# Kernel optimization log

Measured on AMD Instinct MI355X. Metric: run time of the kernel, lower is better.

The kernel has to match this reference:

```python
import jax, jax.numpy as jnp
import numpy as np

N = 100000      # nodes
E = 1600000     # edges
F_IN = 512      # input features
H = 64          # hidden
R = 2           # relations
B = 30          # bases
NEG_SLOPE = 0.2 # GATConv default


def setup_inputs() -> dict:
    key = jax.random.key(0)
    ks = jax.random.split(key, 14)
    s_in = 1.0 / np.sqrt(F_IN)
    s_h = 1.0 / np.sqrt(H)
    return {
        "x": jax.random.normal(ks[0], (N, F_IN), jnp.float32),
        "edge_index": jax.random.randint(ks[1], (2, E), 0, N),
        "edge_types": jax.random.randint(ks[2], (E,), 0, R),
        # RGCN layer 1 (F_IN -> H), basis-decomposed
        "basis1": jax.random.normal(ks[3], (B, F_IN, H), jnp.float32) * s_in,
        "comp1": jax.random.normal(ks[4], (R, B), jnp.float32) * (1.0 / np.sqrt(B)),
        "root1": jax.random.normal(ks[5], (F_IN, H), jnp.float32) * s_in,
        "bias1": jnp.zeros((H,), jnp.float32),
        # RGCN layer 2 (H -> H)
        "basis2": jax.random.normal(ks[6], (B, H, H), jnp.float32) * s_h,
        "comp2": jax.random.normal(ks[7], (R, B), jnp.float32) * (1.0 / np.sqrt(B)),
        "root2": jax.random.normal(ks[8], (H, H), jnp.float32) * s_h,
        "bias2": jnp.zeros((H,), jnp.float32),
        # GAT (H -> 1, heads=1)
        "gat_w": jax.random.normal(ks[9], (H, 1), jnp.float32) * s_h,
        "att_src": jax.random.normal(ks[10], (1,), jnp.float32),
        "att_dst": jax.random.normal(ks[11], (1,), jnp.float32),
        "gat_bias": jnp.zeros((1,), jnp.float32),
    }


def rgcn_layer(x, src, dst, etype, basis, comp, root, bias):
    # W_r = sum_b comp[r,b] * basis[b]; transform nodes once per relation,
    # then gather per edge (math-equal to PyG's per-edge transform, cheaper).
    W = jnp.einsum('rb,bio->rio', comp, basis)       # [R, in, out]
    h = jnp.einsum('ni,rio->rno', x, W)              # [R, N, out]
    out = x @ root + bias                            # root/self term
    for r in range(R):                               # R=2, fixed small loop
        m = (etype == r).astype(x.dtype)             # [E]
        msg = h[r][src] * m[:, None]                 # gather + mask
        agg = jax.ops.segment_sum(msg, dst, num_segments=N)
        cnt = jax.ops.segment_sum(m, dst, num_segments=N)
        out = out + agg / jnp.maximum(cnt, 1.0)[:, None]   # mean aggr per relation
    return out


def gat_layer(x, src, dst, gat_w, att_src, att_dst, gat_bias):
    # GATConv with heads=1, out=1, add_self_loops=True, negative_slope=0.2
    loop = jnp.arange(N)
    s = jnp.concatenate([src, loop])
    d = jnp.concatenate([dst, loop])
    h = x @ gat_w                                    # [N, 1]
    a_s = h[:, 0] * att_src[0]                       # [N]
    a_d = h[:, 0] * att_dst[0]                       # [N]
    e = jax.nn.leaky_relu(a_s[s] + a_d[d], NEG_SLOPE)  # [E+N]
    emax = jax.ops.segment_max(e, d, num_segments=N)   # every dst has self-loop
    ex = jnp.exp(e - emax[d])
    denom = jax.ops.segment_sum(ex, d, num_segments=N)
    alpha = ex / denom[d]                            # segment softmax over dst
    out = jax.ops.segment_sum(alpha[:, None] * h[s], d, num_segments=N)
    return out + gat_bias


def reference(x, edge_index, edge_types,
              basis1, comp1, root1, bias1,
              basis2, comp2, root2, bias2,
              gat_w, att_src, att_dst, gat_bias):
    src, dst = edge_index[0], edge_index[1]
    x1 = jax.nn.relu(rgcn_layer(x, src, dst, edge_types, basis1, comp1, root1, bias1))
    x2 = rgcn_layer(x1, src, dst, edge_types, basis2, comp2, root2, bias2)
    return gat_layer(x2, src, dst, gat_w, att_src, att_dst, gat_bias)  # [N, 1]
```

## Files before the change

### kernel.cpp

```cpp
#include <hip/hip_runtime.h>
#include <hip/hip_bf16.h>
#include <math.h>

#define NCOL 192
#define BB   30
#define SCAN_T 256
#define SCAN_ELEMS 1024

typedef short bf16x8 __attribute__((ext_vector_type(8)));
typedef float f32x4  __attribute__((ext_vector_type(4)));
typedef unsigned short u16x8 __attribute__((ext_vector_type(8)));

__device__ __forceinline__ ushort f2bf(float f) {
  unsigned u = __float_as_uint(f);
  unsigned r = u + 0x7fff + ((u >> 16) & 1);
  return (ushort)(r >> 16);
}
__device__ __forceinline__ float bf2f(ushort u) {
  return __uint_as_float(((unsigned)u) << 16);
}

__global__ void zero_int(int* __restrict__ p, int n) {
  int i = blockIdx.x * blockDim.x + threadIdx.x;
  if (i < n) p[i] = 0;
}

__global__ void hist_deg(const int* __restrict__ dst, int* __restrict__ deg, int E) {
  int e = blockIdx.x * blockDim.x + threadIdx.x;
  if (e >= E) return;
  atomicAdd(&deg[dst[e]], 1);
}

__global__ __launch_bounds__(SCAN_T) void scan_local(const int* __restrict__ deg,
                                                     int* __restrict__ rowptr,
                                                     int* __restrict__ partial, int N) {
  __shared__ int sdata[SCAN_T];
  int t = threadIdx.x;
  int base = blockIdx.x * SCAN_ELEMS + t * 4;
  int v[4], s = 0;
#pragma unroll
  for (int k = 0; k < 4; ++k) {
    v[k] = (base + k < N) ? deg[base + k] : 0;
    s += v[k];
  }
  sdata[t] = s;
  __syncthreads();
  for (int off = 1; off < SCAN_T; off <<= 1) {
    int add = (t >= off) ? sdata[t - off] : 0;
    __syncthreads();
    sdata[t] += add;
    __syncthreads();
  }
  int run = sdata[t] - s;
  if (t == SCAN_T - 1) partial[blockIdx.x] = sdata[t];
#pragma unroll
  for (int k = 0; k < 4; ++k) {
    if (base + k <= N) rowptr[base + k] = run;
    run += v[k];
  }
}

__global__ __launch_bounds__(SCAN_T) void scan_partial(int* __restrict__ partial, int nb) {
  __shared__ int sdata[SCAN_T];
  int t = threadIdx.x;
  int v = (t < nb) ? partial[t] : 0;
  sdata[t] = v;
  __syncthreads();
  for (int off = 1; off < SCAN_T; off <<= 1) {
    int add = (t >= off) ? sdata[t - off] : 0;
    __syncthreads();
    sdata[t] += add;
    __syncthreads();
  }
  if (t < nb) partial[t] = sdata[t] - v;
  if (t == nb - 1) partial[nb] = sdata[t];
}

__global__ void scatter_edges(const int* __restrict__ src, const int* __restrict__ dst,
                              const int* __restrict__ et, const int* __restrict__ rowptr,
                              const int* __restrict__ partial,
                              int* __restrict__ fill, int* __restrict__ srcpk, int E) {
  int e = blockIdx.x * blockDim.x + threadIdx.x;
  if (e >= E) return;
  int d = dst[e];
  int pos = rowptr[d] + partial[d >> 10] + atomicAdd(&fill[d], 1);
  srcpk[pos] = src[e] | (et[e] << 30);
}

__global__ void build_weights(const float* __restrict__ basis1, const float* __restrict__ comp1,
                              const float* __restrict__ root1,
                              const float* __restrict__ basis2, const float* __restrict__ comp2,
                              const float* __restrict__ root2,
                              const float* __restrict__ bias2, const float* __restrict__ gw,
                              ushort* __restrict__ Wpk1, float* __restrict__ w2g,
                              float* __restrict__ cb) {
  int idx = blockIdx.x * blockDim.x + threadIdx.x;
  if (idx < 512 * NCOL) {
    int k = idx / NCOL, j = idx - k * NCOL;
    float v;
    if (j < 64) {
      v = root1[k * 64 + j];
    } else {
      int r = (j >> 6) - 1, o = j & 63;
      float s = 0.f;
#pragma unroll
      for (int b = 0; b < BB; ++b)
        s = fmaf(comp1[r * BB + b], basis1[((size_t)b * 512 + k) * 64 + o], s);
      v = s;
    }
    int chunk = k >> 6, kg = (k >> 3) & 7, elem = k & 7;
    int slot = (kg * NCOL + j) ^ kg;
    Wpk1[(size_t)chunk * 12288 + slot * 8 + elem] = f2bf(v);
    return;
  }
  int widx = idx - 512 * NCOL;
  int c = widx >> 6;
  int o = widx & 63;
  if (c < 192) {
    int k = c & 63, part = c >> 6;
    float s;
    if (part == 0) {
      s = root2[k * 64 + o] * gw[o];
    } else {
      int r = part - 1;
      float t = 0.f;
#pragma unroll
      for (int b = 0; b < BB; ++b)
        t = fmaf(comp2[r * BB + b], basis2[((size_t)b * 64 + k) * 64 + o], t);
      s = t * gw[o];
    }
#pragma unroll
    for (int off = 32; off > 0; off >>= 1) s += __shfl_xor(s, off);
    if (o == 0) w2g[c] = s;
  } else if (c == 192) {
    float s = bias2[o] * gw[o];
#pragma unroll
    for (int off = 32; off > 0; off >>= 1) s += __shfl_xor(s, off);
    if (o == 0) *cb = s;
  }
}

template <int K, int BF16IN>
__global__ __launch_bounds__(256, 3) void gemm_mfma(const void* __restrict__ Xv,
                                                    const ushort* __restrict__ Wpk,
                                                    ushort* __restrict__ Y, int N) {
  constexpr int NC = K / 64;
  constexpr int NB = (NC > 1) ? 2 : 1;
  __shared__ ushort Ws[NB * 12288];

  const int tid  = threadIdx.x;
  const int wid  = tid >> 6;
  const int lane = tid & 63;
  const int lrow = lane & 15;
  const int lhi  = lane >> 4;
  const int row0 = blockIdx.x * 64 + wid * 16;

  int lr = row0 + lrow;
  if (lr >= N) lr = N - 1;
  const float*  Xf = (const float*)Xv  + (size_t)lr * K;
  const ushort* Xh = (const ushort*)Xv + (size_t)lr * K;

#define GLOAD_W(c, buf)                                                        \
  { const ushort* gsrc = Wpk + (size_t)(c) * 12288 + wid * 3072 + lane * 8;    \
    ushort* ldst = Ws + (size_t)(buf) * 12288 + wid * 3072;                    \
    _Pragma("unroll") for (int i = 0; i < 6; ++i)                              \
      __builtin_amdgcn_global_load_lds(                                        \
          (const __attribute__((address_space(1))) unsigned int*)(gsrc + i * 512), \
          (__attribute__((address_space(3))) unsigned int*)(ldst + i * 512),   \
          16, 0, 0); }

  float4 pa[2][4];
  u16x8  ph[2][2];
#define LOAD_A(c, slot)                                                       \
  if constexpr (BF16IN) {                                                     \
    ph[slot][0] = ((const u16x8*)Xh)[(c) * 8 + lhi];                          \
    ph[slot][1] = ((const u16x8*)Xh)[(c) * 8 + 4 + lhi];                      \
  } else {                                                                    \
    _Pragma("unroll") for (int q = 0; q < 4; ++q)                             \
      pa[slot][q] = ((const float4*)Xf)[(c) * 16 + (q >> 1) * 8 + lhi * 2 + (q & 1)]; \
  }
#define MAT_A(slot, tt, areg)                                                 \
  if constexpr (BF16IN) {                                                     \
    areg = (bf16x8)ph[slot][tt];                                              \
  } else {                                                                    \
    float4 v0 = pa[slot][(tt) * 2], v1 = pa[slot][(tt) * 2 + 1];              \
    areg[0] = (short)f2bf(v0.x); areg[1] = (short)f2bf(v0.y);                 \
    areg[2] = (short)f2bf(v0.z); areg[3] = (short)f2bf(v0.w);                 \
    areg[4] = (short)f2bf(v1.x); areg[5] = (short)f2bf(v1.y);                 \
    areg[6] = (short)f2bf(v1.z); areg[7] = (short)f2bf(v1.w);                 \
  }
#define COMP(buf, tt, areg)                                                   \
  { const int kg = (tt) * 4 + lhi;                                            \
    const ushort* ls = Ws + (size_t)(buf) * 12288;                            \
    _Pragma("unroll") for (int h = 0; h < 2; ++h) {                           \
      bf16x8 b[6];                                                            \
      _Pragma("unroll") for (int q = 0; q < 6; ++q) {                         \
        int slot = (kg * NCOL + (h * 6 + q) * 16 + lrow) ^ (kg & 7);          \
        b[q] = *(const bf16x8*)(ls + slot * 8);                               \
      }                                                                       \
      _Pragma("unroll") for (int q = 0; q < 6; ++q)                           \
        acc[h * 6 + q] = __builtin_amdgcn_mfma_f32_16x16x32_bf16(areg, b[q],  \
                                                     acc[h * 6 + q], 0, 0, 0); \
    } }

  GLOAD_W(0, 0)
  LOAD_A(0, 0)
  if constexpr (NC > 1) { LOAD_A(1, 1) }
  __syncthreads();

  f32x4 acc[12];
#pragma unroll
  for (int cc = 0; cc < 12; ++cc) acc[cc] = (f32x4){0.f, 0.f, 0.f, 0.f};

#pragma unroll
  for (int c = 0; c < NC; ++c) {
    if (c + 1 < NC) { GLOAD_W(c + 1, (c + 1) & 1) }
    bf16x8 a0, a1;
    MAT_A(c & 1, 0, a0)
    MAT_A(c & 1, 1, a1)
    if (c + 2 < NC) { LOAD_A(c + 2, c & 1) }
    COMP(NB > 1 ? (c & 1) : 0, 0, a0)
    COMP(NB > 1 ? (c & 1) : 0, 1, a1)
    if (c + 1 < NC) {
      __syncthreads();
    }
  }
#undef GLOAD_W
#undef LOAD_A
#undef MAT_A
#undef COMP

#pragma unroll
  for (int cc = 0; cc < 12; ++cc) {
#pragma unroll
    for (int j = 0; j < 4; ++j) {
      int r = row0 + lhi * 4 + j;
      if (r < N) Y[(size_t)r * NCOL + cc * 16 + lrow] = f2bf(acc[cc][j]);
    }
  }
}

__global__ __launch_bounds__(256) void agg_layer1(const ushort* __restrict__ Y,
                                                  const int* __restrict__ rowptr,
                                                  const int* __restrict__ partial,
                                                  const int* __restrict__ srcpk,
                                                  const float* __restrict__ bias,
                                                  ushort* __restrict__ h1, int N) {
  int n = blockIdx.x * 4 + (threadIdx.x >> 6);
  if (n >= N) return;
  const int lane = threadIdx.x & 63;
  const int g    = lane >> 3;
  const int f0   = (lane & 7) * 8;

  float a0[8], a1[8];
#pragma unroll
  for (int j = 0; j < 8; ++j) { a0[j] = 0.f; a1[j] = 0.f; }
  float c0 = 0.f, c1 = 0.f;

  const int beg = rowptr[n] + partial[n >> 10];
  const int end = rowptr[n + 1] + partial[(n + 1) >> 10];
  for (int i = beg; i < end; i += 16) {
    int eA = i + g, eB = i + 8 + g;
    bool vA = eA < end, vB = eB < end;
    int pkA = 0, pkB = 0;
    if (vA) pkA = srcpk[eA];
    if (vB) pkB = srcpk[eB];
    u16x8 xA = (u16x8){0, 0, 0, 0, 0, 0, 0, 0}, xB = xA;
    if (vA) xA = *(const u16x8*)(Y + (size_t)(pkA & 0x3fffffff) * NCOL + 64 +
                                 ((pkA >> 30) << 6) + f0);
    if (vB) xB = *(const u16x8*)(Y + (size_t)(pkB & 0x3fffffff) * NCOL + 64 +
                                 ((pkB >> 30) << 6) + f0);
    float rA = (vA && (pkA >> 30)) ? 1.f : 0.f;
    float sA = vA ? 1.f : 0.f;
    float rB = (vB && (pkB >> 30)) ? 1.f : 0.f;
    float sB = vB ? 1.f : 0.f;
    c0 += (sA - rA) + (sB - rB);
    c1 += rA + rB;
#pragma unroll
    for (int j = 0; j < 8; ++j) {
      float fA = bf2f(xA[j]), fB = bf2f(xB[j]);
      a0[j] += (sA - rA) * fA + (sB - rB) * fB;
      a1[j] += rA * fA + rB * fB;
    }
  }

#pragma unroll
  for (int msk = 8; msk <= 32; msk <<= 1) {
#pragma unroll
    for (int j = 0; j < 8; ++j) {
      a0[j] += __shfl_xor(a0[j], msk);
      a1[j] += __shfl_xor(a1[j], msk);
    }
    c0 += __shfl_xor(c0, msk);
    c1 += __shfl_xor(c1, msk);
  }

  if (g == 0) {
    float inv0 = 1.f / fmaxf(c0, 1.f);
    float inv1 = 1.f / fmaxf(c1, 1.f);
    u16x8 rv = *(const u16x8*)(Y + (size_t)n * NCOL + f0);
    float4 bA = *(const float4*)(bias + f0);
    float4 bB = *(const float4*)(bias + f0 + 4);
    float bb[8] = {bA.x, bA.y, bA.z, bA.w, bB.x, bB.y, bB.z, bB.w};
    u16x8 o;
#pragma unroll
    for (int j = 0; j < 8; ++j) {
      float v = bf2f(rv[j]) + bb[j] + a0[j] * inv0 + a1[j] * inv1;
      o[j] = f2bf(fmaxf(v, 0.f));
    }
    *(u16x8*)(h1 + (size_t)n * 64 + f0) = o;
  }
}

__global__ __launch_bounds__(256) void agg_layer2(const ushort* __restrict__ h1,
                                                  const int* __restrict__ rowptr,
                                                  const int* __restrict__ partial,
                                                  const int* __restrict__ srcpk,
                                                  const float* __restrict__ w2g,
                                                  const float* __restrict__ cb,
                                                  float* __restrict__ hval, int N) {
  int n = blockIdx.x * 4 + (threadIdx.x >> 6);
  if (n >= N) return;
  const int lane = threadIdx.x & 63;
  const int g    = lane >> 3;
  const int f0   = (lane & 7) * 8;

  float a0[8], a1[8];
#pragma unroll
  for (int j = 0; j < 8; ++j) { a0[j] = 0.f; a1[j] = 0.f; }
  float c0 = 0.f, c1 = 0.f;

  const int beg = rowptr[n] + partial[n >> 10];
  const int end = rowptr[n + 1] + partial[(n + 1) >> 10];
  for (int i = beg; i < end; i += 16) {
    int eA = i + g, eB = i + 8 + g;
    bool vA = eA < end, vB = eB < end;
    int pkA = 0, pkB = 0;
    if (vA) pkA = srcpk[eA];
    if (vB) pkB = srcpk[eB];
    u16x8 xA = (u16x8){0, 0, 0, 0, 0, 0, 0, 0}, xB = xA;
    if (vA) xA = *(const u16x8*)(h1 + (size_t)(pkA & 0x3fffffff) * 64 + f0);
    if (vB) xB = *(const u16x8*)(h1 + (size_t)(pkB & 0x3fffffff) * 64 + f0);
    float rA = (vA && (pkA >> 30)) ? 1.f : 0.f;
    float sA = vA ? 1.f : 0.f;
    float rB = (vB && (pkB >> 30)) ? 1.f : 0.f;
    float sB = vB ? 1.f : 0.f;
    c0 += (sA - rA) + (sB - rB);
    c1 += rA + rB;
#pragma unroll
    for (int j = 0; j < 8; ++j) {
      float fA = bf2f(xA[j]), fB = bf2f(xB[j]);
      a0[j] += (sA - rA) * fA + (sB - rB) * fB;
      a1[j] += rA * fA + rB * fB;
    }
  }

#pragma unroll
  for (int msk = 8; msk <= 32; msk <<= 1) {
#pragma unroll
    for (int j = 0; j < 8; ++j) {
      a0[j] += __shfl_xor(a0[j], msk);
      a1[j] += __shfl_xor(a1[j], msk);
    }
    c0 += __shfl_xor(c0, msk);
    c1 += __shfl_xor(c1, msk);
  }

  float inv0 = 1.f / fmaxf(c0, 1.f);
  float inv1 = 1.f / fmaxf(c1, 1.f);
  u16x8 hv = *(const u16x8*)(h1 + (size_t)n * 64 + f0);
  float4 wA = *(const float4*)(w2g + f0);
  float4 wB = *(const float4*)(w2g + f0 + 4);
  float4 uA = *(const float4*)(w2g + 64 + f0);
  float4 uB = *(const float4*)(w2g + 64 + f0 + 4);
  float4 vA = *(const float4*)(w2g + 128 + f0);
  float4 vB = *(const float4*)(w2g + 128 + f0 + 4);
  float wv[8] = {wA.x, wA.y, wA.z, wA.w, wB.x, wB.y, wB.z, wB.w};
  float uv[8] = {uA.x, uA.y, uA.z, uA.w, uB.x, uB.y, uB.z, uB.w};
  float vv8[8] = {vA.x, vA.y, vA.z, vA.w, vB.x, vB.y, vB.z, vB.w};
  float dot = 0.f;
#pragma unroll
  for (int j = 0; j < 8; ++j) {
    dot = fmaf(bf2f(hv[j]), wv[j], dot);
    dot = fmaf(a0[j] * inv0, uv[j], dot);
    dot = fmaf(a1[j] * inv1, vv8[j], dot);
  }
  dot += __shfl_xor(dot, 1);
  dot += __shfl_xor(dot, 2);
  dot += __shfl_xor(dot, 4);
  if (lane == 0) hval[n] = dot + *cb;
}

__device__ __forceinline__ float leaky(float x) { return x > 0.f ? x : 0.2f * x; }

__global__ __launch_bounds__(256) void gat_csr(const int* __restrict__ rowptr,
                                               const int* __restrict__ partial,
                                               const int* __restrict__ srcpk,
                                               const float* __restrict__ hval,
                                               const float* __restrict__ as_,
                                               const float* __restrict__ ad_,
                                               const float* __restrict__ gb,
                                               float* __restrict__ out, int N) {
  int n = blockIdx.x * 4 + (threadIdx.x >> 6);
  if (n >= N) return;
  const int lane = threadIdx.x & 63;
  float as = *as_, ad = *ad_;
  float hv = hval[n];
  float adn = hv * ad;
  float eself = leaky(hv * as + adn);
  const int beg = rowptr[n] + partial[n >> 10];
  const int end = rowptr[n + 1] + partial[(n + 1) >> 10];
  int deg = end - beg;
  float m, den, acc;
  if (deg <= 64) {
    bool valid = lane < deg;
    float hs = 0.f;
    if (valid) hs = hval[srcpk[beg + lane] & 0x3fffffff];
    float e = valid ? leaky(hs * as + adn) : -3.4e38f;
    m = fmaxf(e, eself);
#pragma unroll
    for (int o = 32; o > 0; o >>= 1) m = fmaxf(m, __shfl_xor(m, o));
    float ex = valid ? expf(e - m) : 0.f;
    den = ex;
    acc = ex * hs;
#pragma unroll
    for (int o = 32; o > 0; o >>= 1) {
      den += __shfl_xor(den, o);
      acc += __shfl_xor(acc, o);
    }
  } else {
    m = eself;
    for (int i = beg + lane; i < end; i += 64)
      m = fmaxf(m, leaky(hval[srcpk[i] & 0x3fffffff] * as + adn));
#pragma unroll
    for (int o = 32; o > 0; o >>= 1) m = fmaxf(m, __shfl_xor(m, o));
    float dl = 0.f, al = 0.f;
    for (int i = beg + lane; i < end; i += 64) {
      float hs = hval[srcpk[i] & 0x3fffffff];
      float ex = expf(leaky(hs * as + adn) - m);
      dl += ex;
      al += ex * hs;
    }
    den = dl;
    acc = al;
#pragma unroll
    for (int o = 32; o > 0; o >>= 1) {
      den += __shfl_xor(den, o);
      acc += __shfl_xor(acc, o);
    }
  }
  float es = expf(eself - m);
  den += es;
  acc += es * hv;
  if (lane == 0) out[n] = acc / den + *gb;
}

extern "C" void kernel_launch(void* const* d_in, const int* in_sizes, int n_in,
                              void* d_out, int out_size, void* d_ws, size_t ws_size,
                              hipStream_t stream) {
  const float* x      = (const float*)d_in[0];
  const int*   eidx   = (const int*)d_in[1];
  const int*   etype  = (const int*)d_in[2];
  const float* basis1 = (const float*)d_in[3];
  const float* comp1  = (const float*)d_in[4];
  const float* root1  = (const float*)d_in[5];
  const float* bias1  = (const float*)d_in[6];
  const float* basis2 = (const float*)d_in[7];
  const float* comp2  = (const float*)d_in[8];
  const float* root2  = (const float*)d_in[9];
  const float* bias2  = (const float*)d_in[10];
  const float* gat_w  = (const float*)d_in[11];
  const float* att_s  = (const float*)d_in[12];
  const float* att_d  = (const float*)d_in[13];
  const float* gat_b  = (const float*)d_in[14];

  const int N = in_sizes[0] / 512;
  const int E = in_sizes[1] / 2;
  const int* src = eidx;
  const int* dst = eidx + E;

  char* p = (char*)d_ws;
  ushort* Y    = (ushort*)p; p += (size_t)N * NCOL * 2;
  ushort* h1   = (ushort*)p; p += (size_t)N * 64 * 2;
  ushort* Wpk1 = (ushort*)p; p += (size_t)512 * NCOL * 2;
  float* w2g   = (float*)p;  p += 192 * 4;
  float* cb    = (float*)p;  p += 16 * 4;
  float* hval  = (float*)p;  p += (size_t)N * 4;
  int* deg     = (int*)p;    p += (size_t)N * 4;
  int* fill    = (int*)p;    p += (size_t)N * 4;
  int* rowptr  = (int*)p;    p += (size_t)(N + 16) * 4;
  int* partial = (int*)p;    p += (size_t)(SCAN_T + 16) * 4;
  int* srcpk   = (int*)p;    p += (size_t)E * 4;
  float* out   = (float*)d_out;

  const int TB = 256;
  const int GB = (N + 63) / 64;
  const int nb = (N + 1 + SCAN_ELEMS - 1) / SCAN_ELEMS;

  zero_int<<<(2 * N + TB - 1) / TB, TB, 0, stream>>>(deg, 2 * N);
  hist_deg<<<(E + TB - 1) / TB, TB, 0, stream>>>(dst, deg, E);
  scan_local<<<nb, SCAN_T, 0, stream>>>(deg, rowptr, partial, N);
  scan_partial<<<1, SCAN_T, 0, stream>>>(partial, nb);
  scatter_edges<<<(E + TB - 1) / TB, TB, 0, stream>>>(src, dst, etype, rowptr, partial,
                                                      fill, srcpk, E);

  build_weights<<<(512 * NCOL + 193 * 64 + TB - 1) / TB, TB, 0, stream>>>(
      basis1, comp1, root1, basis2, comp2, root2, bias2, gat_w, Wpk1, w2g, cb);

  gemm_mfma<512, 0><<<GB, 256, 0, stream>>>(x, Wpk1, Y, N);
  agg_layer1<<<(N + 3) / 4, TB, 0, stream>>>(Y, rowptr, partial, srcpk, bias1, h1, N);

  agg_layer2<<<(N + 3) / 4, TB, 0, stream>>>(h1, rowptr, partial, srcpk, w2g, cb, hval, N);

  gat_csr<<<(N + 3) / 4, TB, 0, stream>>>(rowptr, partial, srcpk, hval, att_s, att_d, gat_b,
                                          out, N);
}
```

Before: 374.3 us.

## Project layer-2 features to scalars before aggregation, aggregate scalars per edge

Layer 2 followed by the GAT projection is linear, so each node's h1 row is first reduced to three scalars: its dot products with the root, relation-0 and relation-1 projected weights. These are computed inside agg_layer1 and stored in small side buffers. The layer-2 aggregation then gathers one float per edge instead of a 64-wide bf16 row, which cuts the gather traffic of that pass. The cost is extra writes and shuffles in agg_layer1. Results also differ slightly because the projection now uses the bf16-rounded h1 before the mean rather than after it.

```diff
diff --git a/kernel.cpp b/kernel.cpp
--- a/kernel.cpp
+++ b/kernel.cpp
@@ -245,7 +245,10 @@
                                                   const int* __restrict__ partial,
                                                   const int* __restrict__ srcpk,
                                                   const float* __restrict__ bias,
-                                                  ushort* __restrict__ h1, int N) {
+                                                  const float* __restrict__ w2g,
+                                                  ushort* __restrict__ h1,
+                                                  float* __restrict__ svf,
+                                                  float* __restrict__ hs, int N) {
   int n = blockIdx.x * 4 + (threadIdx.x >> 6);
   if (n >= N) return;
   const int lane = threadIdx.x & 63;
@@ -302,93 +305,85 @@
     float4 bA = *(const float4*)(bias + f0);
     float4 bB = *(const float4*)(bias + f0 + 4);
     float bb[8] = {bA.x, bA.y, bA.z, bA.w, bB.x, bB.y, bB.z, bB.w};
+    float res[8];
     u16x8 o;
 #pragma unroll
     for (int j = 0; j < 8; ++j) {
       float v = bf2f(rv[j]) + bb[j] + a0[j] * inv0 + a1[j] * inv1;
-      o[j] = f2bf(fmaxf(v, 0.f));
+      res[j] = fmaxf(v, 0.f);
+      o[j] = f2bf(res[j]);
     }
     *(u16x8*)(h1 + (size_t)n * 64 + f0) = o;
-  }
-}
-
-__global__ __launch_bounds__(256) void agg_layer2(const ushort* __restrict__ h1,
-                                                  const int* __restrict__ rowptr,
-                                                  const int* __restrict__ partial,
-                                                  const int* __restrict__ srcpk,
-                                                  const float* __restrict__ w2g,
-                                                  const float* __restrict__ cb,
-                                                  float* __restrict__ hval, int N) {
+
+    float4 wA = *(const float4*)(w2g + f0);
+    float4 wB = *(const float4*)(w2g + f0 + 4);
+    float4 uA = *(const float4*)(w2g + 64 + f0);
+    float4 uB = *(const float4*)(w2g + 64 + f0 + 4);
+    float4 vA4 = *(const float4*)(w2g + 128 + f0);
+    float4 vB4 = *(const float4*)(w2g + 128 + f0 + 4);
+    float wv[8] = {wA.x, wA.y, wA.z, wA.w, wB.x, wB.y, wB.z, wB.w};
+    float uv[8] = {uA.x, uA.y, uA.z, uA.w, uB.x, uB.y, uB.z, uB.w};
+    float vv[8] = {vA4.x, vA4.y, vA4.z, vA4.w, vB4.x, vB4.y, vB4.z, vB4.w};
+    float dw = 0.f, du = 0.f, dv = 0.f;
+#pragma unroll
+    for (int j = 0; j < 8; ++j) {
+      float h = bf2f(o[j]);
+      dw = fmaf(h, wv[j], dw);
+      du = fmaf(h, uv[j], du);
+      dv = fmaf(h, vv[j], dv);
+    }
+#pragma unroll
+    for (int msk = 1; msk <= 4; msk <<= 1) {
+      dw += __shfl_xor(dw, msk);
+      du += __shfl_xor(du, msk);
+      dv += __shfl_xor(dv, msk);
+    }
+    if (lane == 0) {
+      svf[2 * (size_t)n]     = du;
+      svf[2 * (size_t)n + 1] = dv;
+      hs[n] = dw;
+    }
+  }
+}
+
+__global__ __launch_bounds__(256) void agg2_scalar(const int* __restrict__ rowptr,
+                                                   const int* __restrict__ partial,
+                                                   const int* __restrict__ srcpk,
+                                                   const float* __restrict__ svf,
+                                                   const float* __restrict__ hs,
+                                                   const float* __restrict__ cb,
+                                                   float* __restrict__ hval, int N) {
   int n = blockIdx.x * 4 + (threadIdx.x >> 6);
   if (n >= N) return;
   const int lane = threadIdx.x & 63;
-  const int g    = lane >> 3;
-  const int f0   = (lane & 7) * 8;
-
-  float a0[8], a1[8];
-#pragma unroll
-  for (int j = 0; j < 8; ++j) { a0[j] = 0.f; a1[j] = 0.f; }
-  float c0 = 0.f, c1 = 0.f;
-
   const int beg = rowptr[n] + partial[n >> 10];
   const int end = rowptr[n + 1] + partial[(n + 1) >> 10];
-  for (int i = beg; i < end; i += 16) {
-    int eA = i + g, eB = i + 8 + g;
-    bool vA = eA < end, vB = eB < end;
-    int pkA = 0, pkB = 0;
-    if (vA) pkA = srcpk[eA];
-    if (vB) pkB = srcpk[eB];
-    u16x8 xA = (u16x8){0, 0, 0, 0, 0, 0, 0, 0}, xB = xA;
-    if (vA) xA = *(const u16x8*)(h1 + (size_t)(pkA & 0x3fffffff) * 64 + f0);
-    if (vB) xB = *(const u16x8*)(h1 + (size_t)(pkB & 0x3fffffff) * 64 + f0);
-    float rA = (vA && (pkA >> 30)) ? 1.f : 0.f;
-    float sA = vA ? 1.f : 0.f;
-    float rB = (vB && (pkB >> 30)) ? 1.f : 0.f;
-    float sB = vB ? 1.f : 0.f;
-    c0 += (sA - rA) + (sB - rB);
-    c1 += rA + rB;
-#pragma unroll
-    for (int j = 0; j < 8; ++j) {
-      float fA = bf2f(xA[j]), fB = bf2f(xB[j]);
-      a0[j] += (sA - rA) * fA + (sB - rB) * fB;
-      a1[j] += rA * fA + rB * fB;
-    }
-  }
-
-#pragma unroll
-  for (int msk = 8; msk <= 32; msk <<= 1) {
-#pragma unroll
-    for (int j = 0; j < 8; ++j) {
-      a0[j] += __shfl_xor(a0[j], msk);
-      a1[j] += __shfl_xor(a1[j], msk);
-    }
-    c0 += __shfl_xor(c0, msk);
-    c1 += __shfl_xor(c1, msk);
-  }
-
-  float inv0 = 1.f / fmaxf(c0, 1.f);
-  float inv1 = 1.f / fmaxf(c1, 1.f);
-  u16x8 hv = *(const u16x8*)(h1 + (size_t)n * 64 + f0);
-  float4 wA = *(const float4*)(w2g + f0);
-  float4 wB = *(const float4*)(w2g + f0 + 4);
-  float4 uA = *(const float4*)(w2g + 64 + f0);
-  float4 uB = *(const float4*)(w2g + 64 + f0 + 4);
-  float4 vA = *(const float4*)(w2g + 128 + f0);
-  float4 vB = *(const float4*)(w2g + 128 + f0 + 4);
-  float wv[8] = {wA.x, wA.y, wA.z, wA.w, wB.x, wB.y, wB.z, wB.w};
-  float uv[8] = {uA.x, uA.y, uA.z, uA.w, uB.x, uB.y, uB.z, uB.w};
-  float vv8[8] = {vA.x, vA.y, vA.z, vA.w, vB.x, vB.y, vB.z, vB.w};
-  float dot = 0.f;
-#pragma unroll
-  for (int j = 0; j < 8; ++j) {
-    dot = fmaf(bf2f(hv[j]), wv[j], dot);
-    dot = fmaf(a0[j] * inv0, uv[j], dot);
-    dot = fmaf(a1[j] * inv1, vv8[j], dot);
-  }
-  dot += __shfl_xor(dot, 1);
-  dot += __shfl_xor(dot, 2);
-  dot += __shfl_xor(dot, 4);
-  if (lane == 0) hval[n] = dot + *cb;
+  int deg = end - beg;
+  float s0 = 0.f, s1 = 0.f, c0 = 0.f, c1 = 0.f;
+  if (deg <= 64) {
+    if (lane < deg) {
+      int pk = srcpk[beg + lane];
+      int r = pk >> 30;
+      float s = svf[2 * (size_t)(pk & 0x3fffffff) + r];
+      if (r) { s1 = s; c1 = 1.f; } else { s0 = s; c0 = 1.f; }
+    }
+  } else {
+    for (int i = beg + lane; i < end; i += 64) {
+      int pk = srcpk[i];
+      int r = pk >> 30;
+      float s = svf[2 * (size_t)(pk & 0x3fffffff) + r];
+      if (r) { s1 += s; c1 += 1.f; } else { s0 += s; c0 += 1.f; }
+    }
+  }
+#pragma unroll
+  for (int o = 32; o > 0; o >>= 1) {
+    s0 += __shfl_xor(s0, o);
+    s1 += __shfl_xor(s1, o);
+    c0 += __shfl_xor(c0, o);
+    c1 += __shfl_xor(c1, o);
+  }
+  if (lane == 0)
+    hval[n] = hs[n] + s0 / fmaxf(c0, 1.f) + s1 / fmaxf(c1, 1.f) + *cb;
 }
 
 __device__ __forceinline__ float leaky(float x) { return x > 0.f ? x : 0.2f * x; }
@@ -486,6 +481,8 @@
   float* w2g   = (float*)p;  p += 192 * 4;
   float* cb    = (float*)p;  p += 16 * 4;
   float* hval  = (float*)p;  p += (size_t)N * 4;
+  float* svf   = (float*)p;  p += (size_t)N * 2 * 4;
+  float* hs    = (float*)p;  p += (size_t)N * 4;
   int* deg     = (int*)p;    p += (size_t)N * 4;
   int* fill    = (int*)p;    p += (size_t)N * 4;
   int* rowptr  = (int*)p;    p += (size_t)(N + 16) * 4;
@@ -508,9 +505,10 @@
       basis1, comp1, root1, basis2, comp2, root2, bias2, gat_w, Wpk1, w2g, cb);
 
   gemm_mfma<512, 0><<<GB, 256, 0, stream>>>(x, Wpk1, Y, N);
-  agg_layer1<<<(N + 3) / 4, TB, 0, stream>>>(Y, rowptr, partial, srcpk, bias1, h1, N);
-
-  agg_layer2<<<(N + 3) / 4, TB, 0, stream>>>(h1, rowptr, partial, srcpk, w2g, cb, hval, N);
+  agg_layer1<<<(N + 3) / 4, TB, 0, stream>>>(Y, rowptr, partial, srcpk, bias1, w2g,
+                                             h1, svf, hs, N);
+
+  agg2_scalar<<<(N + 3) / 4, TB, 0, stream>>>(rowptr, partial, srcpk, svf, hs, cb, hval, N);
 
   gat_csr<<<(N + 3) / 4, TB, 0, stream>>>(rowptr, partial, srcpk, hval, att_s, att_d, gat_b,
                                           out, N);
```

After: 349.4 us (median of 3 runs). 1.07x faster.
